# Performance work log

Measured on AMD Instinct MI355X. Metric: run time of the kernel, lower is better.

## Reference

```python
import jax, jax.numpy as jnp
import numpy as np

Q, M, B, D, H, DH, DI = 512, 512, 8, 1024, 16, 64, 4096
K = Q + M  # klen = rlen


def layer_norm(x, g, b, eps=1e-5):
    mu = x.mean(-1, keepdims=True)
    var = ((x - mu) ** 2).mean(-1, keepdims=True)
    return (x - mu) / jnp.sqrt(var + eps) * g + b


def rel_shift(x):
    # x: [qlen, klen, bsz, n_heads] -> Transformer-XL relative shift
    q, k = x.shape[0], x.shape[1]
    zero_pad = jnp.zeros((q, 1) + x.shape[2:], x.dtype)
    x_padded = jnp.concatenate([zero_pad, x], axis=1)          # [q, k+1, b, n]
    x_padded = x_padded.reshape((k + 1, q) + x.shape[2:])       # row-major reinterpret
    return x_padded[1:].reshape(x.shape)


def setup_inputs() -> dict:
    key = jax.random.key(0)
    ks = jax.random.split(key, 12)
    rn = lambda k, s: jax.random.normal(k, s, jnp.float32)
    # causal mask with memory: query i (absolute pos i+M) cannot attend to key j > i+M
    i = jnp.arange(Q)[:, None]
    j = jnp.arange(K)[None, :]
    attn_mask = (j > (i + M))[:, :, None]  # [Q, K, 1] bool
    return dict(
        w=rn(ks[0], (Q, B, D)),
        r=rn(ks[1], (K, D)),
        r_w_bias=rn(ks[2], (H, DH)) * 0.02,
        r_r_bias=rn(ks[3], (H, DH)) * 0.02,
        mems=rn(ks[4], (M, B, D)),
        attn_mask=attn_mask,
        Wqkv=rn(ks[5], (3 * H * DH, D)) * 0.02,
        Wr=rn(ks[6], (H * DH, D)) * 0.02,
        Wo=rn(ks[7], (D, H * DH)) * 0.02,
        ln1_g=jnp.ones(D), ln1_b=jnp.zeros(D),
        W1=rn(ks[8], (DI, D)) * 0.02, b1=jnp.zeros(DI),
        W2=rn(ks[9], (D, DI)) * 0.02, b2=jnp.zeros(D),
        ln2_g=jnp.ones(D), ln2_b=jnp.zeros(D),
    )


def reference(w, r, r_w_bias, r_r_bias, mems, attn_mask,
              Wqkv, Wr, Wo, ln1_g, ln1_b, W1, b1, W2, b2, ln2_g, ln2_b):
    qlen, bsz = w.shape[0], w.shape[1]
    scale = 1.0 / (DH ** 0.5)

    cat = jnp.concatenate([mems, w], axis=0)                 # [K, B, D]
    heads = cat @ Wqkv.T                                     # [K, B, 3*H*DH] (post-lnorm: no LN here)
    q, k, v = jnp.split(heads, 3, axis=-1)
    q = q[-qlen:]                                            # [Q, B, H*DH]
    r_k = r @ Wr.T                                           # [K, H*DH]

    klen = k.shape[0]
    q = q.reshape(qlen, bsz, H, DH)
    k = k.reshape(klen, bsz, H, DH)
    v = v.reshape(klen, bsz, H, DH)
    r_k = r_k.reshape(klen, H, DH)

    AC = jnp.einsum('ibnd,jbnd->ijbn', q + r_w_bias, k)      # content score
    BD = rel_shift(jnp.einsum('ibnd,jnd->ijbn', q + r_r_bias, r_k))  # position score
    attn_score = (AC + BD) * scale                           # [Q, K, B, H]
    attn_score = jnp.where(attn_mask[:, :, :, None], -jnp.inf, attn_score)

    attn_prob = jax.nn.softmax(attn_score, axis=1)
    attn_vec = jnp.einsum('ijbn,jbnd->ibnd', attn_prob, v)
    attn_vec = attn_vec.reshape(qlen, bsz, H * DH)
    attn_out = attn_vec @ Wo.T
    out1 = layer_norm(w + attn_out, ln1_g, ln1_b)            # post-lnorm residual

    ff = jax.nn.relu(out1 @ W1.T + b1) @ W2.T + b2           # position-wise FFN
    out = layer_norm(out1 + ff, ln2_g, ln2_b)
    return out
```

## Files before the change

### kernel.cpp

```cpp
#include <hip/hip_runtime.h>
#include <hip/hip_bf16.h>

typedef __hip_bfloat16 bf16;

typedef __attribute__((ext_vector_type(8))) short frag8;
typedef __attribute__((ext_vector_type(4))) float f32x4;

__device__ __forceinline__ bf16 f2bf(float f) { return __float2bfloat16(f); }

__device__ __forceinline__ float u16f(unsigned short u) {
  union { unsigned int i; float f; } c; c.i = ((unsigned int)u) << 16; return c.f;
}
__device__ __forceinline__ unsigned short bfbits(float f) {
  union { bf16 b; unsigned short u; } c; c.b = __float2bfloat16(f); return c.u;
}
__device__ __forceinline__ float tof(float x) { return x; }
__device__ __forceinline__ float tof(bf16 x)  { return __bfloat162float(x); }

__device__ __forceinline__ void gload_lds16(const bf16* g, short* l) {
  __builtin_amdgcn_global_load_lds(
      (const __attribute__((address_space(1))) void*)g,
      (__attribute__((address_space(3))) void*)l, 16, 0, 0);
}

#define EP_PLAIN 0
#define EP_QKV   1
#define EP_RK    2

struct CvtArgs {
  const float* src[8];
  bf16* dst[8];
  int cum[9];
};
__global__ __launch_bounds__(256)
void cvt8(CvtArgs a)
{
  const int i = blockIdx.x * 256 + threadIdx.x;
  if (i >= a.cum[8]) return;
  int seg = 7;
  #pragma unroll
  for (int s2 = 6; s2 >= 0; --s2) if (i < a.cum[s2 + 1]) seg = s2;
  const int o = i - a.cum[seg];
  float4 v = ((const float4*)a.src[seg])[o];
  ushort4 u;
  u.x = bfbits(v.x); u.y = bfbits(v.y); u.z = bfbits(v.z); u.w = bfbits(v.w);
  ((ushort4*)a.dst[seg])[o] = u;
}

template<typename TRES>
__global__ __launch_bounds__(256)
void mgemm(const bf16* __restrict__ A, const bf16* __restrict__ W,
           const float* __restrict__ bias, const TRES* __restrict__ res,
           bf16* __restrict__ out,
           bf16* __restrict__ qwb, bf16* __restrict__ qrb,
           bf16* __restrict__ kbo, bf16* __restrict__ vto,
           const float* __restrict__ rwbias, const float* __restrict__ rrbias,
           int M, int N, int K, int mode, int relu)
{
  __shared__ __align__(16) short sA[2][128 * 32];
  __shared__ __align__(16) short sB[2][128 * 32];
  const int tid  = threadIdx.x;
  const int lane = tid & 63;
  const int wave = tid >> 6;
  const int quad = lane >> 4;
  const int l15  = lane & 15;
  const int m0 = blockIdx.y * 128;
  const int n0 = blockIdx.x * 128;
  const int wm = (wave >> 1) * 64;
  const int wn = (wave & 1) * 64;

  const int lr = tid >> 2;
  const int lc = (tid & 3) << 3;

  const bf16* aptr0 = A + (size_t)(m0 + lr) * K + lc;
  const bf16* aptr1 = aptr0 + (size_t)64 * K;
  const bf16* wptr0 = W + (size_t)(n0 + lr) * K + lc;
  const bf16* wptr1 = wptr0 + (size_t)64 * K;

  f32x4 acc[4][4] = {};

  auto stage = [&](int buf, int kk) {
    gload_lds16(aptr0 + kk, &sA[buf][wave * 512]);
    gload_lds16(aptr1 + kk, &sA[buf][2048 + wave * 512]);
    gload_lds16(wptr0 + kk, &sB[buf][wave * 512]);
    gload_lds16(wptr1 + kk, &sB[buf][2048 + wave * 512]);
  };

  stage(0, 0);
  __syncthreads();
  int cur = 0;

  for (int kk = 0; kk < K; kk += 32) {
    if (kk + 32 < K) stage(cur ^ 1, kk + 32);
    frag8 af[4], bfr[4];
    #pragma unroll
    for (int t = 0; t < 4; ++t) {
      af[t]  = *(const frag8*)&sA[cur][(wm + t * 16 + l15) * 32 + quad * 8];
      bfr[t] = *(const frag8*)&sB[cur][(wn + t * 16 + l15) * 32 + quad * 8];
    }
    #pragma unroll
    for (int mi = 0; mi < 4; ++mi)
      #pragma unroll
      for (int ni = 0; ni < 4; ++ni)
        acc[mi][ni] = __builtin_amdgcn_mfma_f32_16x16x32_bf16(
            af[mi], bfr[ni], acc[mi][ni], 0, 0, 0);
    __syncthreads();
    cur ^= 1;
  }

  #pragma unroll
  for (int mi = 0; mi < 4; ++mi) {
    #pragma unroll
    for (int reg = 0; reg < 4; ++reg) {
      const int row = m0 + wm + mi * 16 + quad * 4 + reg;
      if (mode == EP_PLAIN) {
        bf16* orow = out + (size_t)row * N;
        const TRES* rrow = res ? res + (size_t)row * N : nullptr;
        #pragma unroll
        for (int ni = 0; ni < 4; ++ni) {
          const int col = n0 + wn + ni * 16 + l15;
          float v = acc[mi][ni][reg];
          if (bias) v += bias[col];
          if (relu) v = fmaxf(v, 0.f);
          if (rrow) v += tof(rrow[col]);
          orow[col] = f2bf(v);
        }
      } else if (mode == EP_QKV) {
        const int t = row >> 3, bb = row & 7;
        #pragma unroll
        for (int ni = 0; ni < 4; ++ni) {
          const int col = n0 + wn + ni * 16 + l15;
          const float v = acc[mi][ni][reg];
          const int seg = col >> 10;
          const int cl  = col & 1023;
          const int hn  = cl >> 6, d = cl & 63;
          if (seg == 0) {
            if (t >= 512) {
              const size_t idx = (((size_t)bb * 16 + hn) * 512 + (t - 512)) * 64 + d;
              qwb[idx] = f2bf(v + rwbias[cl]);
              qrb[idx] = f2bf(v + rrbias[cl]);
            }
          } else if (seg == 1) {
            kbo[(((size_t)bb * 16 + hn) * 1024 + t) * 64 + d] = f2bf(v);
          } else {
            vto[(((size_t)bb * 16 + hn) * 64 + d) * 1024 + t] = f2bf(v);
          }
        }
      } else {
        #pragma unroll
        for (int ni = 0; ni < 4; ++ni) {
          const int col = n0 + wn + ni * 16 + l15;
          const int hn = col >> 6, d = col & 63;
          qwb[((size_t)hn * 1024 + row) * 64 + d] = f2bf(acc[mi][ni][reg]);
        }
      }
    }
  }
}

__global__ __launch_bounds__(256, 3)
void fattn(const bf16* __restrict__ qw, const bf16* __restrict__ qr,
           const bf16* __restrict__ kb, const bf16* __restrict__ vT,
           const bf16* __restrict__ rk, bf16* __restrict__ avec)
{
  __shared__ __align__(16) short sK[8192];
  __shared__ __align__(16) short sV[8192];
  __shared__ __align__(16) unsigned short p_lds[4][16][136];
  const int tid  = threadIdx.x;
  const int wave = tid >> 6, lane = tid & 63;
  const int quad = lane >> 4, l15 = lane & 15;
  const int bid = blockIdx.x;
  const int r_  = bid & 7;
  const int s_  = bid >> 3;
  const int phi = s_ & 15;
  const int it  = s_ >> 4;
  const int pr  = r_ + 8 * phi;
  const int h   = pr & 15;
  const int b   = pr >> 4;
  const int i0  = it * 64;
  const int iw  = i0 + wave * 16;
  const size_t bh = (size_t)b * 16 + h;
  const bf16* kp = kb + bh * 1024 * 64;
  const bf16* vp = vT + bh * 64 * 1024;
  const bf16* rp = rk + (size_t)h * 1024 * 64;

  frag8 aqw[2], aqr[2];
  {
    const bf16* r0 = qw + (bh * 512 + iw + l15) * 64 + quad * 8;
    aqw[0] = *(const frag8*)r0;
    aqw[1] = *(const frag8*)(r0 + 32);
    const bf16* r1 = qr + (bh * 512 + iw + l15) * 64 + quad * 8;
    aqr[0] = *(const frag8*)r1;
    aqr[1] = *(const frag8*)(r1 + 32);
  }

  f32x4 accO[4] = {};
  float m_run[4], l_run[4];
  #pragma unroll
  for (int rg = 0; rg < 4; ++rg) { m_run[rg] = -INFINITY; l_run[rg] = 0.f; }

  const int nsteps = ((i0 + 63 + 512) >> 7) + 1;
  const int offb   = 15 + l15 - quad * 4;

  auto stage = [&](int j0s) {
    #pragma unroll
    for (int c = 0; c < 4; ++c) {
      const int Lb  = c * 4096 + tid * 16;
      short* ldst   = (short*)((char*)sK + (c * 4096 + wave * 1024));
      short* ldstV  = (short*)((char*)sV + (c * 4096 + wave * 1024));
      const int rK  = Lb >> 7;
      const int UK  = Lb ^ ((rK & 7) << 4);
      gload_lds16((const bf16*)((const char*)kp + (size_t)j0s * 128 + UK), ldst);
      const int rV  = Lb >> 8;
      const int UV  = Lb ^ ((rV & 7) << 4);
      const int cbV = UV & 255;
      gload_lds16((const bf16*)((const char*)vp + (size_t)rV * 2048 + (size_t)j0s * 2 + cbV),
                  ldstV);
    }
  };
  stage(0);

  for (int jt = 0; jt < nsteps; ++jt) {
    const int j0 = jt << 7;
    const int pbase = 496 + j0 - iw;
    f32x4 bsub[9];
    #pragma unroll
    for (int ns = 0; ns < 9; ++ns) {
      const int prow = min(pbase + ns * 16 + l15, 1023);
      const bf16* rrow = rp + (size_t)prow * 64 + quad * 8;
      frag8 br0 = *(const frag8*)rrow;
      frag8 br1 = *(const frag8*)(rrow + 32);
      f32x4 z = {};
      z = __builtin_amdgcn_mfma_f32_16x16x32_bf16(aqr[0], br0, z, 0,0,0);
      bsub[ns] = __builtin_amdgcn_mfma_f32_16x16x32_bf16(aqr[1], br1, z, 0,0,0);
    }
    __syncthreads();
    f32x4 accS[8] = {};
    #pragma unroll
    for (int ns = 0; ns < 8; ++ns) {
      const int row = ns * 16 + l15;
      const int sw  = (row & 7) << 4;
      frag8 bk0 = *(const frag8*)((const char*)sK + ((row * 128 + quad * 16) ^ sw));
      frag8 bk1 = *(const frag8*)((const char*)sK + ((row * 128 + 64 + quad * 16) ^ sw));
      accS[ns] = __builtin_amdgcn_mfma_f32_16x16x32_bf16(aqw[0], bk0, accS[ns], 0,0,0);
      accS[ns] = __builtin_amdgcn_mfma_f32_16x16x32_bf16(aqw[1], bk1, accS[ns], 0,0,0);
    }
    float tmax[4] = {-INFINITY, -INFINITY, -INFINITY, -INFINITY};
    #pragma unroll
    for (int ns = 0; ns < 8; ++ns) {
      #pragma unroll
      for (int rg = 0; rg < 4; ++rg) {
        const int o    = offb - rg;
        const int srcl = (quad << 4) | (o & 15);
        const float lo = __shfl(bsub[ns][rg],     srcl, 64);
        const float hi = __shfl(bsub[ns + 1][rg], srcl, 64);
        const float bd = (o & 16) ? hi : lo;
        float s = (accS[ns][rg] + bd) * 0.125f;
        const int j = j0 + ns * 16 + l15;
        s = (j > iw + quad * 4 + rg + 512) ? -INFINITY : s;
        accS[ns][rg] = s;
        tmax[rg] = fmaxf(tmax[rg], s);
      }
    }
    #pragma unroll
    for (int off = 1; off < 16; off <<= 1)
      #pragma unroll
      for (int rg = 0; rg < 4; ++rg)
        tmax[rg] = fmaxf(tmax[rg], __shfl_xor(tmax[rg], off, 64));
    float alpha[4], tsum[4] = {0.f, 0.f, 0.f, 0.f};
    #pragma unroll
    for (int rg = 0; rg < 4; ++rg) {
      const float nm = fmaxf(m_run[rg], tmax[rg]);
      alpha[rg] = __expf(m_run[rg] - nm);
      m_run[rg] = nm;
    }
    #pragma unroll
    for (int ns = 0; ns < 8; ++ns)
      #pragma unroll
      for (int rg = 0; rg < 4; ++rg) {
        const int rl = quad * 4 + rg;
        const float pv = __expf(accS[ns][rg] - m_run[rg]);
        tsum[rg] += pv;
        p_lds[wave][rl][ns * 16 + l15] = bfbits(pv);
      }
    #pragma unroll
    for (int off = 1; off < 16; off <<= 1)
      #pragma unroll
      for (int rg = 0; rg < 4; ++rg)
        tsum[rg] += __shfl_xor(tsum[rg], off, 64);
    #pragma unroll
    for (int rg = 0; rg < 4; ++rg)
      l_run[rg] = l_run[rg] * alpha[rg] + tsum[rg];
    #pragma unroll
    for (int nd = 0; nd < 4; ++nd)
      #pragma unroll
      for (int rg = 0; rg < 4; ++rg)
        accO[nd][rg] *= alpha[rg];
    __builtin_amdgcn_wave_barrier();
    #pragma unroll
    for (int ks = 0; ks < 4; ++ks) {
      frag8 ap = *(const frag8*)&p_lds[wave][l15][ks * 32 + quad * 8];
      #pragma unroll
      for (int nd = 0; nd < 4; ++nd) {
        const int d = nd * 16 + l15;
        frag8 bv = *(const frag8*)((const char*)sV +
                    ((d * 256 + ks * 64 + quad * 16) ^ ((d & 7) << 4)));
        accO[nd] = __builtin_amdgcn_mfma_f32_16x16x32_bf16(ap, bv, accO[nd], 0,0,0);
      }
    }
    __builtin_amdgcn_wave_barrier();
    __syncthreads();
    if (jt + 1 < nsteps) stage((jt + 1) << 7);
  }

  #pragma unroll
  for (int rg = 0; rg < 4; ++rg) {
    const int i = iw + quad * 4 + rg;
    const float inv = 1.f / l_run[rg];
    #pragma unroll
    for (int nd = 0; nd < 4; ++nd) {
      const int d = nd * 16 + l15;
      avec[((size_t)i * 8 + b) * 1024 + h * 64 + d] = f2bf(accO[nd][rg] * inv);
    }
  }
}

template<typename TOUT>
__global__ __launch_bounds__(256)
void ln_kernel(const bf16* __restrict__ x, const float* __restrict__ g,
               const float* __restrict__ be, TOUT* __restrict__ out)
{
  __shared__ float red0[4];
  __shared__ float red1[4];
  const int row = blockIdx.x;
  const int tid = threadIdx.x;
  const bf16* xr = x + (size_t)row * 1024;
  ushort4 u = *(const ushort4*)(xr + (tid << 2));
  const float v0 = u16f(u.x), v1 = u16f(u.y), v2 = u16f(u.z), v3 = u16f(u.w);
  float sum = v0 + v1 + v2 + v3;
  #pragma unroll
  for (int off = 1; off < 64; off <<= 1) sum += __shfl_xor(sum, off, 64);
  if ((tid & 63) == 0) red0[tid >> 6] = sum;
  __syncthreads();
  const float mu = (red0[0] + red0[1] + red0[2] + red0[3]) * (1.f / 1024.f);
  const float d0 = v0 - mu, d1 = v1 - mu, d2 = v2 - mu, d3 = v3 - mu;
  float sq = d0*d0 + d1*d1 + d2*d2 + d3*d3;
  #pragma unroll
  for (int off = 1; off < 64; off <<= 1) sq += __shfl_xor(sq, off, 64);
  if ((tid & 63) == 0) red1[tid >> 6] = sq;
  __syncthreads();
  const float var = (red1[0] + red1[1] + red1[2] + red1[3]) * (1.f / 1024.f);
  const float inv = 1.f / sqrtf(var + 1e-5f);
  const int c = tid << 2;
  float4 ug = *(const float4*)(g + c);
  float4 ub = *(const float4*)(be + c);
  TOUT* orow = out + (size_t)row * 1024;
  orow[c+0] = (TOUT)(d0 * inv * ug.x + ub.x);
  orow[c+1] = (TOUT)(d1 * inv * ug.y + ub.y);
  orow[c+2] = (TOUT)(d2 * inv * ug.z + ub.z);
  orow[c+3] = (TOUT)(d3 * inv * ug.w + ub.w);
}

extern "C" void kernel_launch(void* const* d_in, const int* in_sizes, int n_in,
                              void* d_out, int out_size, void* d_ws, size_t ws_size,
                              hipStream_t stream)
{
  const float* w    = (const float*)d_in[0];
  const float* r    = (const float*)d_in[1];
  const float* rwb  = (const float*)d_in[2];
  const float* rrb  = (const float*)d_in[3];
  const float* mems = (const float*)d_in[4];
  const float* Wqkv = (const float*)d_in[6];
  const float* Wr   = (const float*)d_in[7];
  const float* Wo   = (const float*)d_in[8];
  const float* ln1g = (const float*)d_in[9];
  const float* ln1b = (const float*)d_in[10];
  const float* W1   = (const float*)d_in[11];
  const float* b1   = (const float*)d_in[12];
  const float* W2   = (const float*)d_in[13];
  const float* b2   = (const float*)d_in[14];
  const float* ln2g = (const float*)d_in[15];
  const float* ln2b = (const float*)d_in[16];

  const size_t MB = 1u << 20;
  char* p = (char*)d_ws;
  bf16* catb  = (bf16*)(p +  0 * MB);
  bf16* wqkvb = (bf16*)(p + 16 * MB);
  bf16* wrb   = (bf16*)(p + 22 * MB);
  bf16* wob   = (bf16*)(p + 24 * MB);
  bf16* w1b   = (bf16*)(p + 26 * MB);
  bf16* w2b   = (bf16*)(p + 34 * MB);
  bf16* qwbuf = (bf16*)(p + 42 * MB);
  bf16* qrbuf = (bf16*)(p + 50 * MB);
  bf16* kbuf  = (bf16*)(p + 58 * MB);
  bf16* vTbuf = (bf16*)(p + 74 * MB);
  bf16* rkbuf = (bf16*)(p + 90 * MB);
  bf16* rb    = (bf16*)(p + 92 * MB);
  bf16* avec  = (bf16*)(p +  0 * MB);
  bf16* x1    = (bf16*)(p +  8 * MB);
  bf16* o1    = (bf16*)(p + 42 * MB);
  bf16* x2    = (bf16*)(p + 50 * MB);
  bf16* h     = (bf16*)(p + 58 * MB);

  dim3 blk(256);
  {
    CvtArgs a;
    const int n4w = (4096 * 1024) / 4, n4r = (1024 * 1024) / 4,
              n4qkv = (3072 * 1024) / 4;
    a.src[0] = mems; a.dst[0] = catb;                        int n0_ = n4w;
    a.src[1] = w;    a.dst[1] = catb + (size_t)4096 * 1024;  int n1_ = n4w;
    a.src[2] = r;    a.dst[2] = rb;                          int n2_ = n4r;
    a.src[3] = Wqkv; a.dst[3] = wqkvb;                       int n3_ = n4qkv;
    a.src[4] = Wr;   a.dst[4] = wrb;                         int n4_ = n4r;
    a.src[5] = Wo;   a.dst[5] = wob;                         int n5_ = n4r;
    a.src[6] = W1;   a.dst[6] = w1b;                         int n6_ = n4w;
    a.src[7] = W2;   a.dst[7] = w2b;                         int n7_ = n4w;
    const int ns_[8] = {n0_, n1_, n2_, n3_, n4_, n5_, n6_, n7_};
    a.cum[0] = 0;
    for (int s2 = 0; s2 < 8; ++s2) a.cum[s2 + 1] = a.cum[s2] + ns_[s2];
    cvt8<<<dim3((a.cum[8] + 255) / 256), blk, 0, stream>>>(a);
  }

  mgemm<float><<<dim3(24, 64), blk, 0, stream>>>(catb, wqkvb, nullptr, (const float*)nullptr,
        nullptr, qwbuf, qrbuf, kbuf, vTbuf, rwb, rrb, 8192, 3072, 1024, EP_QKV, 0);
  mgemm<float><<<dim3(8, 8), blk, 0, stream>>>(rb, wrb, nullptr, (const float*)nullptr,
        nullptr, rkbuf, nullptr, nullptr, nullptr, nullptr, nullptr,
        1024, 1024, 1024, EP_RK, 0);
  fattn<<<dim3(1024), blk, 0, stream>>>(qwbuf, qrbuf, kbuf, vTbuf, rkbuf, avec);
  mgemm<float><<<dim3(8, 32), blk, 0, stream>>>(avec, wob, nullptr, w,
        x1, nullptr, nullptr, nullptr, nullptr, nullptr, nullptr,
        4096, 1024, 1024, EP_PLAIN, 0);
  ln_kernel<bf16><<<dim3(4096), blk, 0, stream>>>(x1, ln1g, ln1b, o1);
  mgemm<float><<<dim3(32, 32), blk, 0, stream>>>(o1, w1b, b1, (const float*)nullptr,
        h, nullptr, nullptr, nullptr, nullptr, nullptr, nullptr,
        4096, 4096, 1024, EP_PLAIN, 1);
  mgemm<bf16><<<dim3(8, 32), blk, 0, stream>>>(h, w2b, b2, o1,
        x2, nullptr, nullptr, nullptr, nullptr, nullptr, nullptr,
        4096, 1024, 4096, EP_PLAIN, 0);
  ln_kernel<float><<<dim3(4096), blk, 0, stream>>>(x2, ln2g, ln2b, (float*)d_out);
}
```

Measured before the change: 604.1 us.

## Split QKV GEMM to skip unused Q rows and transpose V through LDS

The fused QKV projection previously computed Q for all 1024 positions and discarded the memory half. It is now split into a K/V GEMM over all rows and a Q GEMM over only the last 512 rows, which removes about a sixth of the projection FLOPs. The V epilogue now stages the tile in shared memory with an XOR swizzle so the transposed V layout can be written as contiguous 16-element vectors instead of strided scalar stores. The cost is one extra kernel launch and an LDS round trip plus barrier in the V epilogue.

After: 556.1 us. 8.0% less time.

```diff
diff --git a/kernel.cpp b/kernel.cpp
--- a/kernel.cpp
+++ b/kernel.cpp
@@ -24,8 +24,9 @@
 }
 
 #define EP_PLAIN 0
-#define EP_QKV   1
 #define EP_RK    2
+#define EP_Q     3
+#define EP_KV    4
 
 struct CvtArgs {
   const float* src[8];
@@ -57,8 +58,9 @@
            const float* __restrict__ rwbias, const float* __restrict__ rrbias,
            int M, int N, int K, int mode, int relu)
 {
-  __shared__ __align__(16) short sA[2][128 * 32];
-  __shared__ __align__(16) short sB[2][128 * 32];
+  __shared__ __align__(16) short smem[16384];
+  short (*sA)[4096] = reinterpret_cast<short(*)[4096]>(smem);
+  short (*sB)[4096] = reinterpret_cast<short(*)[4096]>(smem + 8192);
   const int tid  = threadIdx.x;
   const int lane = tid & 63;
   const int wave = tid >> 6;
@@ -108,11 +110,51 @@
     cur ^= 1;
   }
 
+  if (mode == EP_KV && n0 >= 1024) {
+    #pragma unroll
+    for (int mi = 0; mi < 4; ++mi) {
+      #pragma unroll
+      for (int reg = 0; reg < 4; ++reg) {
+        const int rowl = wm + mi * 16 + quad * 4 + reg;
+        const int bbl  = rowl & 7;
+        const int tl   = rowl >> 3;
+        #pragma unroll
+        for (int ni = 0; ni < 4; ++ni) {
+          const int coll = wn + ni * 16 + l15;
+          const int hn2  = coll >> 6;
+          const int d    = coll & 63;
+          const int rowid = (bbl * 2 + hn2) * 64 + d;
+          smem[tl * 1024 + (rowid ^ (tl << 1))] =
+              (short)bfbits(acc[mi][ni][reg]);
+        }
+      }
+    }
+    __syncthreads();
+    const int hnb = (n0 >> 6) - 16;
+    const int t0  = m0 >> 3;
+    #pragma unroll
+    for (int p = 0; p < 4; ++p) {
+      const int r   = p * 256 + tid;
+      const int bbl = r >> 7;
+      const int hn2 = (r >> 6) & 1;
+      const int d   = r & 63;
+      unsigned short tmp[16];
+      #pragma unroll
+      for (int tl = 0; tl < 16; ++tl)
+        tmp[tl] = (unsigned short)smem[tl * 1024 + (r ^ (tl << 1))];
+      bf16* dst = vto + ((size_t)(bbl * 16 + hnb + hn2) * 64 + d) * 1024 + t0;
+      *(frag8*)dst       = *(const frag8*)&tmp[0];
+      *(frag8*)(dst + 8) = *(const frag8*)&tmp[8];
+    }
+    return;
+  }
+
   #pragma unroll
   for (int mi = 0; mi < 4; ++mi) {
     #pragma unroll
     for (int reg = 0; reg < 4; ++reg) {
-      const int row = m0 + wm + mi * 16 + quad * 4 + reg;
+      const int rowl = wm + mi * 16 + quad * 4 + reg;
+      const int row  = m0 + rowl;
       if (mode == EP_PLAIN) {
         bf16* orow = out + (size_t)row * N;
         const TRES* rrow = res ? res + (size_t)row * N : nullptr;
@@ -125,26 +167,25 @@
           if (rrow) v += tof(rrow[col]);
           orow[col] = f2bf(v);
         }
-      } else if (mode == EP_QKV) {
+      } else if (mode == EP_KV) {
         const int t = row >> 3, bb = row & 7;
         #pragma unroll
         for (int ni = 0; ni < 4; ++ni) {
           const int col = n0 + wn + ni * 16 + l15;
+          const int hn = col >> 6, d = col & 63;
+          kbo[((size_t)(bb * 16 + hn) * 1024 + t) * 64 + d] =
+              f2bf(acc[mi][ni][reg]);
+        }
+      } else if (mode == EP_Q) {
+        const int tq = row >> 3, bb = row & 7;
+        #pragma unroll
+        for (int ni = 0; ni < 4; ++ni) {
+          const int col = n0 + wn + ni * 16 + l15;
+          const int hn = col >> 6, d = col & 63;
           const float v = acc[mi][ni][reg];
-          const int seg = col >> 10;
-          const int cl  = col & 1023;
-          const int hn  = cl >> 6, d = cl & 63;
-          if (seg == 0) {
-            if (t >= 512) {
-              const size_t idx = (((size_t)bb * 16 + hn) * 512 + (t - 512)) * 64 + d;
-              qwb[idx] = f2bf(v + rwbias[cl]);
-              qrb[idx] = f2bf(v + rrbias[cl]);
-            }
-          } else if (seg == 1) {
-            kbo[(((size_t)bb * 16 + hn) * 1024 + t) * 64 + d] = f2bf(v);
-          } else {
-            vto[(((size_t)bb * 16 + hn) * 64 + d) * 1024 + t] = f2bf(v);
-          }
+          const size_t idx = ((size_t)(bb * 16 + hn) * 512 + tq) * 64 + d;
+          qwb[idx] = f2bf(v + rwbias[col]);
+          qrb[idx] = f2bf(v + rrbias[col]);
         }
       } else {
         #pragma unroll
@@ -421,8 +462,12 @@
     cvt8<<<dim3((a.cum[8] + 255) / 256), blk, 0, stream>>>(a);
   }
 
-  mgemm<float><<<dim3(24, 64), blk, 0, stream>>>(catb, wqkvb, nullptr, (const float*)nullptr,
-        nullptr, qwbuf, qrbuf, kbuf, vTbuf, rwb, rrb, 8192, 3072, 1024, EP_QKV, 0);
+  mgemm<float><<<dim3(16, 64), blk, 0, stream>>>(catb, wqkvb + (size_t)1024 * 1024,
+        nullptr, (const float*)nullptr, nullptr, nullptr, nullptr, kbuf, vTbuf,
+        nullptr, nullptr, 8192, 2048, 1024, EP_KV, 0);
+  mgemm<float><<<dim3(8, 32), blk, 0, stream>>>(catb + (size_t)4096 * 1024, wqkvb,
+        nullptr, (const float*)nullptr, nullptr, qwbuf, qrbuf, nullptr, nullptr,
+        rwb, rrb, 4096, 1024, 1024, EP_Q, 0);
   mgemm<float><<<dim3(8, 8), blk, 0, stream>>>(rb, wrb, nullptr, (const float*)nullptr,
         nullptr, rkbuf, nullptr, nullptr, nullptr, nullptr, nullptr,
         1024, 1024, 1024, EP_RK, 0);
```
